# Kernel tuning notes

Hardware: AMD Instinct MI355X
Metric: run time of the kernel (lower is better)

The kernel has to match this reference:

```python
import jax, jax.numpy as jnp
import numpy as np

N = 30000        # nodes
E = 300000       # edges (before self-loops)
B = 300          # graphs
EMB = 64         # emb_dim (inner_dim overwritten to emb_dim in __init__)
HEADS = 4
OUT3 = 121       # hard-coded in conv3
H3 = 6           # heads of conv3
NCLS = 10
NVOC = 5000      # node token vocab for node_encoder
MAXD = 64        # max node depth for node_encoder


def _p(k, shape, scale=0.1):
    return scale * jax.random.normal(k, shape, dtype=jnp.float32)


def setup_inputs() -> dict:
    key = jax.random.key(0)
    ks = jax.random.split(key, 20)
    inp = {}
    inp["x"] = jax.random.randint(ks[0], (N, 1), 0, NVOC, dtype=jnp.int32)
    inp["node_depth"] = jax.random.randint(ks[1], (N, 1), 0, MAXD, dtype=jnp.int32)
    inp["edge_index"] = jax.random.randint(ks[2], (2, E), 0, N, dtype=jnp.int32)
    inp["batch"] = jnp.sort(jax.random.randint(ks[3], (N,), 0, B, dtype=jnp.int32))
    # node_encoder params (token emb + depth emb)
    inp["node_emb"] = _p(ks[4], (NVOC, EMB))
    inp["depth_emb"] = _p(ks[5], (MAXD, EMB))
    d1 = HEADS * EMB
    inp["w1"] = _p(ks[6], (EMB, d1))
    inp["as1"] = _p(ks[7], (HEADS, EMB))
    inp["ad1"] = _p(ks[8], (HEADS, EMB))
    inp["b1"] = jnp.zeros((d1,), jnp.float32)
    inp["w2"] = _p(ks[9], (d1, d1))
    inp["as2"] = _p(ks[10], (HEADS, EMB))
    inp["ad2"] = _p(ks[11], (HEADS, EMB))
    inp["b2"] = jnp.zeros((d1,), jnp.float32)
    d3 = H3 * OUT3
    inp["w3"] = _p(ks[12], (d1, d3))
    inp["as3"] = _p(ks[13], (H3, OUT3))
    inp["ad3"] = _p(ks[14], (H3, OUT3))
    inp["b3"] = jnp.zeros((d3,), jnp.float32)
    inp["wp"] = _p(ks[15], (OUT3, NCLS))
    inp["bp"] = jnp.zeros((NCLS,), jnp.float32)
    return inp


def gat_conv(x, W, a_src, a_dst, bias, src, dst, heads, out_dim):
    """PyG GATConv (concat=True, self-loops already in src/dst)."""
    n = x.shape[0]
    h = (x @ W).reshape(n, heads, out_dim)          # [N,H,D]
    es = (h * a_src).sum(-1)                        # [N,H] per-node src logits
    ed = (h * a_dst).sum(-1)                        # [N,H]
    e = jax.nn.leaky_relu(es[src] + ed[dst], 0.2)   # [E,H]
    # segment softmax over destination nodes (every node has a self-loop)
    m = jax.ops.segment_max(e, dst, num_segments=n)
    ex = jnp.exp(e - m[dst])
    s = jax.ops.segment_sum(ex, dst, num_segments=n)
    alpha = ex / (s[dst] + 1e-16)                   # [E,H]
    out = jax.ops.segment_sum(h[src] * alpha[:, :, None], dst, num_segments=n)
    return out.reshape(n, heads * out_dim) + bias


def reference(x, node_depth, edge_index, batch, node_emb, depth_emb,
              w1, as1, ad1, b1, w2, as2, ad2, b2, w3, as3, ad3, b3, wp, bp):
    n = x.shape[0]
    loops = jnp.arange(n, dtype=edge_index.dtype)
    src = jnp.concatenate([edge_index[0], loops])
    dst = jnp.concatenate([edge_index[1], loops])
    # node_encoder: token embedding + depth embedding
    h = node_emb[x[:, 0]] + depth_emb[node_depth.reshape(-1)]
    h = jax.nn.elu(gat_conv(h, w1, as1, ad1, b1, src, dst, HEADS, EMB))
    h = jax.nn.elu(gat_conv(h, w2, as2, ad2, b2, src, dst, HEADS, EMB))
    h = gat_conv(h, w3, as3, ad3, b3, src, dst, H3, OUT3)   # [N, 726]
    # global mean pool over graphs
    sums = jax.ops.segment_sum(h, batch, num_segments=B)
    cnt = jax.ops.segment_sum(jnp.ones((n,), h.dtype), batch, num_segments=B)
    g = sums / jnp.maximum(cnt, 1.0)[:, None]               # [B, 726]
    g = g.reshape(-1, H3, OUT3).mean(axis=1)                # [B, 121]
    return g @ wp + bp                                      # [B, NCLS]
```

## Files before the change

### kernel.cpp

```cpp
#include <hip/hip_runtime.h>
#include <hip/hip_bf16.h>
#include <math.h>

#define NN   30000
#define NE   300000
#define ETOT 330000
#define NB   300
#define EMB  64
#define D1   256
#define H1   4
#define H3   6
#define O3   121
#define D3   726
#define NQ   60
#define N3   72
#define NCLS 10
#define CAP  64
#define LDA  40

typedef __attribute__((ext_vector_type(8))) short short8;
typedef __attribute__((ext_vector_type(8))) unsigned short ushort8;
typedef __attribute__((ext_vector_type(4))) float floatx4;

static inline int ceil_div(int a, int b) { return (a + b - 1) / b; }

__device__ inline void split_bf16(float f, unsigned short& hi, unsigned short& lo) {
    __hip_bfloat16 h = __float2bfloat16(f);
    float fh = __bfloat162float(h);
    __hip_bfloat16 l = __float2bfloat16(f - fh);
    hi = __builtin_bit_cast(unsigned short, h);
    lo = __builtin_bit_cast(unsigned short, l);
}

__device__ inline float bf2f(unsigned short u) {
    return __builtin_bit_cast(float, (unsigned int)u << 16);
}

__device__ inline unsigned short f2bf(float f) {
    return __builtin_bit_cast(unsigned short, __float2bfloat16(f));
}

__device__ inline float lrelu(float v) { return v > 0.f ? v : 0.2f * v; }


__global__ void setup_kernel(const int* __restrict__ x, const int* __restrict__ dep,
                             const int* __restrict__ ei, const int* __restrict__ batch,
                             const float* __restrict__ nemb, const float* __restrict__ demb,
                             const float* __restrict__ w1, const float* __restrict__ w2,
                             const float* __restrict__ w3, const float* __restrict__ as3,
                             const float* __restrict__ ad3, const float* __restrict__ wp,
                             const float* __restrict__ b3,
                             unsigned short* __restrict__ H0hi, unsigned short* __restrict__ H0lo,
                             unsigned short* __restrict__ W1hi, unsigned short* __restrict__ W1lo,
                             unsigned short* __restrict__ W2b, unsigned short* __restrict__ W3b,
                             float* __restrict__ btv,
                             int* __restrict__ cnt, int* __restrict__ csr,
                             int* __restrict__ gs, int* __restrict__ ge) {
    int i = blockIdx.x * blockDim.x + threadIdx.x;
    if (i < NN * EMB) {
        int n = i >> 6, d = i & 63;
        float v = nemb[x[n] * EMB + d] + demb[dep[n] * EMB + d];
        split_bf16(v, H0hi[i], H0lo[i]);
    }
    if (i < ETOT) {
        int src, dst;
        if (i < NE) { src = ei[i]; dst = ei[NE + i]; }
        else        { src = i - NE; dst = src; }
        int slot = atomicAdd(&cnt[dst], 1);
        csr[dst * CAP + slot] = src;
    }
    if (i < NN) {
        int b = batch[i];
        if (i == 0 || batch[i - 1] != b) gs[b] = i;
        if (i == NN - 1 || batch[i + 1] != b) ge[b] = i + 1;
    }
    if (i < EMB * D1) {
        int k = i / D1, n = i % D1;
        unsigned short h, l;
        split_bf16(w1[i], h, l);
        W1hi[n * EMB + k] = h;
        W1lo[n * EMB + k] = l;
    }
    if (i < D1 * D1) {
        int k = i / D1, n = i % D1;
        W2b[n * D1 + k] = f2bf(w2[i]);
    }
    if (i < N3 * D1 * 8) {
        int oid = i >> 3, sub = i & 7;
        int n = oid / D1, k = oid % D1;
        const float* wrow = w3 + (size_t)k * D3;
        float acc = 0.f;
        if (n < NQ) {
            int h = n / NCLS, c = n % NCLS;
            const float* wr = wrow + h * O3;
            for (int j = sub; j < O3; j += 8) acc += wr[j] * wp[j * NCLS + c];
        } else if (n < NQ + H3) {
            int h = n - NQ;
            const float* wr = wrow + h * O3;
            for (int j = sub; j < O3; j += 8) acc += wr[j] * as3[h * O3 + j];
        } else {
            int h = n - NQ - H3;
            const float* wr = wrow + h * O3;
            for (int j = sub; j < O3; j += 8) acc += wr[j] * ad3[h * O3 + j];
        }
        acc += __shfl_xor(acc, 1);
        acc += __shfl_xor(acc, 2);
        acc += __shfl_xor(acc, 4);
        if (sub == 0) W3b[oid] = f2bf(acc);
    }
    if (i < NCLS * 8) {
        int c = i >> 3, sub = i & 7;
        float acc = 0.f;
        for (int k = sub; k < O3; k += 8) {
            float bs = 0.f;
            #pragma unroll
            for (int hh = 0; hh < H3; hh++) bs += b3[hh * O3 + k];
            acc += bs * wp[k * NCLS + c];
        }
        acc += __shfl_xor(acc, 1);
        acc += __shfl_xor(acc, 2);
        acc += __shfl_xor(acc, 4);
        if (sub == 0) btv[c] = acc;
    }
}


template <int MODE, bool SPLIT>
__global__ __launch_bounds__(256) void gemm_mfma_kernel(
    const unsigned short* __restrict__ Ahi, const unsigned short* __restrict__ Alo,
    const unsigned short* __restrict__ Bhi, const unsigned short* __restrict__ Blo,
    unsigned short* __restrict__ Cbf, unsigned short* __restrict__ Qb,
    float* __restrict__ es, float* __restrict__ ed,
    const float* __restrict__ as_, const float* __restrict__ ad_,
    int M, int K, int N) {
    __shared__ unsigned short sAh[128 * LDA], sBh[128 * LDA];
    __shared__ unsigned short sAl[SPLIT ? 128 * LDA : 1], sBl[SPLIT ? 128 * LDA : 1];
    int tid = threadIdx.x;
    int lane = tid & 63, wave = tid >> 6;
    int wr = (wave >> 1) * 64, wc = (wave & 1) * 64;
    int quad = lane >> 4, mr = lane & 15;
    int row0 = blockIdx.y * 128, col0 = blockIdx.x * 128;

    floatx4 zero = {0.f, 0.f, 0.f, 0.f};
    floatx4 acc[4][4];
    #pragma unroll
    for (int i = 0; i < 4; i++)
        #pragma unroll
        for (int j = 0; j < 4; j++) acc[i][j] = zero;

    for (int k0 = 0; k0 < K; k0 += 32) {
        #pragma unroll
        for (int ch = 0; ch < 2; ch++) {
            int linear = (ch * 256 + tid) * 8;
            int r = linear >> 5, c = linear & 31;
            uint4 vh, vl;
            int gr = row0 + r;
            if (gr < M) {
                vh = *(const uint4*)(Ahi + (size_t)gr * K + k0 + c);
                if (SPLIT) vl = *(const uint4*)(Alo + (size_t)gr * K + k0 + c);
            } else { vh = uint4{0, 0, 0, 0}; vl = uint4{0, 0, 0, 0}; }
            *(uint4*)&sAh[r * LDA + c] = vh;
            if (SPLIT) *(uint4*)&sAl[r * LDA + c] = vl;
            int gn = col0 + r;
            if (gn < N) {
                vh = *(const uint4*)(Bhi + (size_t)gn * K + k0 + c);
                if (SPLIT) vl = *(const uint4*)(Blo + (size_t)gn * K + k0 + c);
            } else { vh = uint4{0, 0, 0, 0}; vl = uint4{0, 0, 0, 0}; }
            *(uint4*)&sBh[r * LDA + c] = vh;
            if (SPLIT) *(uint4*)&sBl[r * LDA + c] = vl;
        }
        __syncthreads();

        short8 ah[4], al[4], bh[4], bl[4];
        #pragma unroll
        for (int i = 0; i < 4; i++) {
            int ar = wr + i * 16 + mr;
            ah[i] = *(const short8*)&sAh[ar * LDA + quad * 8];
            if (SPLIT) al[i] = *(const short8*)&sAl[ar * LDA + quad * 8];
            int br = wc + i * 16 + mr;
            bh[i] = *(const short8*)&sBh[br * LDA + quad * 8];
            if (SPLIT) bl[i] = *(const short8*)&sBl[br * LDA + quad * 8];
        }
        #pragma unroll
        for (int i = 0; i < 4; i++)
            #pragma unroll
            for (int j = 0; j < 4; j++) {
                acc[i][j] = __builtin_amdgcn_mfma_f32_16x16x32_bf16(ah[i], bh[j], acc[i][j], 0, 0, 0);
                if (SPLIT) {
                    acc[i][j] = __builtin_amdgcn_mfma_f32_16x16x32_bf16(ah[i], bl[j], acc[i][j], 0, 0, 0);
                    acc[i][j] = __builtin_amdgcn_mfma_f32_16x16x32_bf16(al[i], bh[j], acc[i][j], 0, 0, 0);
                }
            }
        __syncthreads();
    }

    #pragma unroll
    for (int i = 0; i < 4; i++) {
        #pragma unroll
        for (int j = 0; j < 4; j++) {
            int gc = col0 + wc + j * 16 + mr;
            if (gc >= N) continue;
            int gr0 = row0 + wr + i * 16 + quad * 4;
            #pragma unroll
            for (int r = 0; r < 4; r++) {
                int gr = gr0 + r;
                if (gr >= M) continue;
                float v = acc[i][j][r];
                if (MODE == 0) {
                    Cbf[(size_t)gr * D1 + gc] = f2bf(v);
                } else {
                    if (gc < NQ)            Qb[(size_t)gr * NQ + gc] = f2bf(v);
                    else if (gc < NQ + H3)  es[(size_t)gr * H3 + (gc - NQ)] = v;
                    else                    ed[(size_t)gr * H3 + (gc - NQ - H3)] = v;
                }
            }
        }
    }

    if (MODE == 0) {
        int hx = 2 * blockIdx.x + (wave & 1);
        float asr[4], adr[4];
        #pragma unroll
        for (int j = 0; j < 4; j++) {
            asr[j] = as_[hx * 64 + j * 16 + mr];
            adr[j] = ad_[hx * 64 + j * 16 + mr];
        }
        #pragma unroll
        for (int i = 0; i < 4; i++) {
            #pragma unroll
            for (int r = 0; r < 4; r++) {
                float ps = 0.f, pd = 0.f;
                #pragma unroll
                for (int j = 0; j < 4; j++) {
                    float v = acc[i][j][r];
                    ps += v * asr[j];
                    pd += v * adr[j];
                }
                #pragma unroll
                for (int m2 = 8; m2 >= 1; m2 >>= 1) {
                    ps += __shfl_xor(ps, m2);
                    pd += __shfl_xor(pd, m2);
                }
                int gr = row0 + wr + i * 16 + quad * 4 + r;
                if (mr == 0 && gr < M) {
                    es[gr * 4 + hx] = ps;
                    ed[gr * 4 + hx] = pd;
                }
            }
        }
    }
}


__global__ __launch_bounds__(256) void aggregate12_kernel(
    const unsigned short* __restrict__ P, const float* __restrict__ es,
    const float* __restrict__ ed, const int* __restrict__ cnt,
    const int* __restrict__ csr, const float* __restrict__ bias,
    unsigned short* __restrict__ outHi) {
    int wave = threadIdx.x >> 6, lane = threadIdx.x & 63;
    int wid = blockIdx.x * 4 + wave;
    int hi = lane >> 5;
    int fl = lane & 31;
    int hq = fl >> 3;
    int f0 = fl * 8;
    float bv[8];
    #pragma unroll
    for (int j = 0; j < 8; j++) bv[j] = bias[f0 + j];
    #pragma unroll 1
    for (int t = 0; t < 4; t++) {
        int dst = wid * 4 + t;
        int s0 = dst * CAP, s1 = s0 + cnt[dst];
        float edv = ed[dst * 4 + hq];
        float sum = 0.f;
        float acc[8];
        #pragma unroll
        for (int j = 0; j < 8; j++) acc[j] = 0.f;
        int s = s0;
        for (; s + 8 <= s1; s += 8) {
            int si[4]; float ev[4]; ushort8 pp[4];
            #pragma unroll
            for (int u = 0; u < 4; u++) si[u] = csr[s + 2 * u + hi];
            #pragma unroll
            for (int u = 0; u < 4; u++) {
                ev[u] = es[si[u] * 4 + hq] + edv;
                pp[u] = *(const ushort8*)(P + (size_t)si[u] * D1 + f0);
            }
            #pragma unroll
            for (int u = 0; u < 4; u++) {
                float e = __expf(lrelu(ev[u]));
                sum += e;
                #pragma unroll
                for (int j = 0; j < 8; j++) acc[j] += e * bf2f(pp[u][j]);
            }
        }
        for (; s + 4 <= s1; s += 4) {
            int si[2]; float ev[2]; ushort8 pp[2];
            #pragma unroll
            for (int u = 0; u < 2; u++) si[u] = csr[s + 2 * u + hi];
            #pragma unroll
            for (int u = 0; u < 2; u++) {
                ev[u] = es[si[u] * 4 + hq] + edv;
                pp[u] = *(const ushort8*)(P + (size_t)si[u] * D1 + f0);
            }
            #pragma unroll
            for (int u = 0; u < 2; u++) {
                float e = __expf(lrelu(ev[u]));
                sum += e;
                #pragma unroll
                for (int j = 0; j < 8; j++) acc[j] += e * bf2f(pp[u][j]);
            }
        }
        for (; s < s1; s += 2) {
            int idx = s + hi;
            bool v = idx < s1;
            int si = csr[v ? idx : s];
            float evv = es[si * 4 + hq] + edv;
            ushort8 p8 = *(const ushort8*)(P + (size_t)si * D1 + f0);
            float e = v ? __expf(lrelu(evv)) : 0.f;
            sum += e;
            #pragma unroll
            for (int j = 0; j < 8; j++) acc[j] += e * bf2f(p8[j]);
        }
        sum += __shfl_xor(sum, 32);
        #pragma unroll
        for (int j = 0; j < 8; j++) acc[j] += __shfl_xor(acc[j], 32);
        float inv = 1.f / sum;
        if (lane < 32) {
            ushort8 o8;
            #pragma unroll
            for (int j = 0; j < 8; j++) {
                float a = acc[j] * inv + bv[j];
                a = a > 0.f ? a : expm1f(a);
                o8[j] = f2bf(a);
            }
            *(ushort8*)(outHi + (size_t)dst * D1 + f0) = o8;
        }
    }
}


__global__ __launch_bounds__(256) void aggregate3q_kernel(
    const unsigned short* __restrict__ Qb, const float* __restrict__ es,
    const float* __restrict__ ed, const int* __restrict__ cnt,
    const int* __restrict__ csr, const int* __restrict__ batch,
    float* __restrict__ G,
    const int* __restrict__ gs, const int* __restrict__ ge,
    const float* __restrict__ btv, const float* __restrict__ bp,
    float* __restrict__ out, int* __restrict__ bar) {
    __shared__ int s_last;
    int wave = threadIdx.x >> 6, lane = threadIdx.x & 63;
    int wid = blockIdx.x * 4 + wave;
    bool act = lane < NQ;
    int h = act ? (lane / NCLS) : 0;
    int q = act ? lane : 0;
    #pragma unroll 1
    for (int t = 0; t < 4; t++) {
        int dst = wid * 4 + t;
        int b = batch[dst];
        int s0 = dst * CAP, s1 = s0 + cnt[dst];
        float edv = act ? ed[dst * H3 + h] : 0.f;
        float sum = 0.f, acc = 0.f;
        int s = s0;
        for (; s + 8 <= s1; s += 8) {
            int si[8];
            #pragma unroll
            for (int u = 0; u < 8; u++) si[u] = csr[s + u];
            float vv[8], qq[8];
            #pragma unroll
            for (int u = 0; u < 8; u++) {
                vv[u] = es[si[u] * H3 + h] + edv;
                qq[u] = bf2f(Qb[(size_t)si[u] * NQ + q]);
            }
            #pragma unroll
            for (int u = 0; u < 8; u++) {
                float e = __expf(lrelu(vv[u]));
                sum += e;
                acc += e * qq[u];
            }
        }
        for (; s + 2 <= s1; s += 2) {
            int sa = csr[s], sb = csr[s + 1];
            float va = es[sa * H3 + h] + edv;
            float vb = es[sb * H3 + h] + edv;
            float qa = bf2f(Qb[(size_t)sa * NQ + q]);
            float qb = bf2f(Qb[(size_t)sb * NQ + q]);
            float ea = __expf(lrelu(va));
            float eb = __expf(lrelu(vb));
            sum += ea + eb;
            acc += ea * qa + eb * qb;
        }
        for (; s < s1; s++) {
            int sa = csr[s];
            float va = es[sa * H3 + h] + edv;
            float qa = bf2f(Qb[(size_t)sa * NQ + q]);
            float ea = __expf(lrelu(va));
            sum += ea;
            acc += ea * qa;
        }
        acc *= 1.f / sum;
        float av = act ? acc : 0.f;
        float tot = av;
        #pragma unroll
        for (int h2 = 1; h2 < H3; h2++) tot += __shfl(av, lane + h2 * NCLS);
        if (lane < NCLS) atomicAdd(&G[b * NCLS + lane], tot);
    }

    asm volatile("s_waitcnt vmcnt(0)" ::: "memory");
    __syncthreads();
    if (threadIdx.x == 0) {
        int old = atomicAdd(bar, 1);
        int last = (old == (int)gridDim.x - 1) ? 1 : 0;
        if (last) __threadfence();
        s_last = last;
    }
    __syncthreads();
    if (s_last) {
        for (int i = threadIdx.x; i < NB * NCLS; i += blockDim.x) {
            int b = i / NCLS, c = i % NCLS;
            int cntn = ge[b] - gs[b];
            float o = bp[c];
            if (cntn > 0)
                o += G[i] / (6.f * (float)cntn) + btv[c] * (1.f / 6.f);
            out[i] = o;
        }
    }
}


extern "C" void kernel_launch(void* const* d_in, const int* in_sizes, int n_in,
                              void* d_out, int out_size, void* d_ws, size_t ws_size,
                              hipStream_t stream) {
    const int* x     = (const int*)d_in[0];
    const int* dep   = (const int*)d_in[1];
    const int* ei    = (const int*)d_in[2];
    const int* batch = (const int*)d_in[3];
    const float* nemb = (const float*)d_in[4];
    const float* demb = (const float*)d_in[5];
    const float* w1  = (const float*)d_in[6];
    const float* as1 = (const float*)d_in[7];
    const float* ad1 = (const float*)d_in[8];
    const float* b1  = (const float*)d_in[9];
    const float* w2  = (const float*)d_in[10];
    const float* as2 = (const float*)d_in[11];
    const float* ad2 = (const float*)d_in[12];
    const float* b2  = (const float*)d_in[13];
    const float* w3  = (const float*)d_in[14];
    const float* as3 = (const float*)d_in[15];
    const float* ad3 = (const float*)d_in[16];
    const float* b3  = (const float*)d_in[17];
    const float* wp  = (const float*)d_in[18];
    const float* bp  = (const float*)d_in[19];
    float* out = (float*)d_out;

    char* ws = (char*)d_ws;
    size_t off = 0;
    auto alloc = [&](size_t bytes) -> void* {
        void* p = ws + off;
        off += (bytes + 255) & ~(size_t)255;
        return p;
    };
    unsigned short* Hb   = (unsigned short*)alloc((size_t)NN * D1 * 2);
    unsigned short* H0lo = (unsigned short*)alloc((size_t)NN * EMB * 2);
    unsigned short* W1hi = (unsigned short*)alloc((size_t)D1 * EMB * 2);
    unsigned short* W1lo = (unsigned short*)alloc((size_t)D1 * EMB * 2);
    unsigned short* W2b  = (unsigned short*)alloc((size_t)D1 * D1 * 2);
    unsigned short* W3b  = (unsigned short*)alloc((size_t)N3 * D1 * 2);
    unsigned short* Pb   = (unsigned short*)alloc((size_t)NN * D1 * 2);
    unsigned short* Qb   = (unsigned short*)alloc(((size_t)NN * NQ + 64) * 2);
    float* es   = (float*)alloc((size_t)NN * 6 * 4);
    float* ed   = (float*)alloc((size_t)NN * 6 * 4);
    int* csr    = (int*)alloc((size_t)NN * CAP * 4);
    float* btv  = (float*)alloc((size_t)NCLS * 4);
    char* zstart = ws + off;
    float* G    = (float*)alloc((size_t)NB * NCLS * 4);
    int* gs     = (int*)alloc((size_t)NB * 4);
    int* ge     = (int*)alloc((size_t)NB * 4);
    int* cnt    = (int*)alloc((size_t)NN * 4);
    int* bar    = (int*)alloc((size_t)64 * 4);
    size_t zbytes = (size_t)((ws + off) - zstart);

    hipMemsetAsync(zstart, 0, zbytes, stream);

    setup_kernel<<<ceil_div(NN * EMB, 256), 256, 0, stream>>>(
        x, dep, ei, batch, nemb, demb, w1, w2, w3, as3, ad3, wp, b3,
        Hb, H0lo, W1hi, W1lo, W2b, W3b, btv, cnt, csr, gs, ge);

    gemm_mfma_kernel<0, true><<<dim3(2, ceil_div(NN, 128)), 256, 0, stream>>>(
        Hb, H0lo, W1hi, W1lo, Pb, nullptr, es, ed, as1, ad1, NN, EMB, D1);
    aggregate12_kernel<<<NN / 16, 256, 0, stream>>>(Pb, es, ed, cnt, csr, b1, Hb);

    gemm_mfma_kernel<0, false><<<dim3(2, ceil_div(NN, 128)), 256, 0, stream>>>(
        Hb, nullptr, W2b, nullptr, Pb, nullptr, es, ed, as2, ad2, NN, D1, D1);
    aggregate12_kernel<<<NN / 16, 256, 0, stream>>>(Pb, es, ed, cnt, csr, b2, Hb);

    gemm_mfma_kernel<1, false><<<dim3(1, ceil_div(NN, 128)), 256, 0, stream>>>(
        Hb, nullptr, W3b, nullptr, nullptr, Qb, es, ed, nullptr, nullptr, NN, D1, N3);

    aggregate3q_kernel<<<NN / 16, 256, 0, stream>>>(
        Qb, es, ed, cnt, csr, batch, G, gs, ge, btv, bp, out, bar);
}
```

Measured before the change: 278.1 us.

## Prefetch next node's CSR indices into lanes and shuffle-broadcast neighbor ids

In both aggregation kernels, each lane now loads one neighbor index of the destination node's CSR row into a register, and per-edge source ids are obtained by lane shuffles instead of repeated global loads. The degree, ed value and index row for the next destination node are prefetched during the current one, so that latency overlaps with the gather work. The three unrolled remainder loops are replaced by one masked loop of 8 edges, which removes tail code but spends loads and exps on masked lanes for the last partial block.

```diff
diff --git a/kernel.cpp b/kernel.cpp
--- a/kernel.cpp
+++ b/kernel.cpp
@@ -266,60 +266,49 @@
     float bv[8];
     #pragma unroll
     for (int j = 0; j < 8; j++) bv[j] = bias[f0 + j];
+
+    int dstN = wid * 4;
+    int degN = cnt[dstN];
+    float edvN = ed[dstN * 4 + hq];
+    int sivN = csr[dstN * CAP + (fl < degN ? fl : degN - 1)];
+
     #pragma unroll 1
     for (int t = 0; t < 4; t++) {
-        int dst = wid * 4 + t;
-        int s0 = dst * CAP, s1 = s0 + cnt[dst];
-        float edv = ed[dst * 4 + hq];
+        int dst = dstN;
+        int deg = degN;
+        float edv = edvN;
+        int siv = sivN;
+        if (t < 3) {
+            dstN = dst + 1;
+            degN = cnt[dstN];
+            edvN = ed[dstN * 4 + hq];
+            sivN = csr[dstN * CAP + (fl < degN ? fl : degN - 1)];
+        }
         float sum = 0.f;
         float acc[8];
         #pragma unroll
         for (int j = 0; j < 8; j++) acc[j] = 0.f;
-        int s = s0;
-        for (; s + 8 <= s1; s += 8) {
-            int si[4]; float ev[4]; ushort8 pp[4];
-            #pragma unroll
-            for (int u = 0; u < 4; u++) si[u] = csr[s + 2 * u + hi];
+        #pragma unroll 1
+        for (int sb = 0; sb < deg; sb += 8) {
+            float ev[4]; ushort8 pp[4]; bool vm[4];
             #pragma unroll
             for (int u = 0; u < 4; u++) {
-                ev[u] = es[si[u] * 4 + hq] + edv;
-                pp[u] = *(const ushort8*)(P + (size_t)si[u] * D1 + f0);
+                int e = sb + 2 * u + hi;
+                bool v = e < deg;
+                vm[u] = v;
+                int si;
+                if (e < 32) si = __shfl(siv, v ? e : 0);
+                else        si = csr[dst * CAP + (v ? e : 0)];
+                ev[u] = es[si * 4 + hq] + edv;
+                pp[u] = *(const ushort8*)(P + (size_t)si * D1 + f0);
             }
             #pragma unroll
             for (int u = 0; u < 4; u++) {
-                float e = __expf(lrelu(ev[u]));
+                float e = vm[u] ? __expf(lrelu(ev[u])) : 0.f;
                 sum += e;
                 #pragma unroll
                 for (int j = 0; j < 8; j++) acc[j] += e * bf2f(pp[u][j]);
             }
-        }
-        for (; s + 4 <= s1; s += 4) {
-            int si[2]; float ev[2]; ushort8 pp[2];
-            #pragma unroll
-            for (int u = 0; u < 2; u++) si[u] = csr[s + 2 * u + hi];
-            #pragma unroll
-            for (int u = 0; u < 2; u++) {
-                ev[u] = es[si[u] * 4 + hq] + edv;
-                pp[u] = *(const ushort8*)(P + (size_t)si[u] * D1 + f0);
-            }
-            #pragma unroll
-            for (int u = 0; u < 2; u++) {
-                float e = __expf(lrelu(ev[u]));
-                sum += e;
-                #pragma unroll
-                for (int j = 0; j < 8; j++) acc[j] += e * bf2f(pp[u][j]);
-            }
-        }
-        for (; s < s1; s += 2) {
-            int idx = s + hi;
-            bool v = idx < s1;
-            int si = csr[v ? idx : s];
-            float evv = es[si * 4 + hq] + edv;
-            ushort8 p8 = *(const ushort8*)(P + (size_t)si * D1 + f0);
-            float e = v ? __expf(lrelu(evv)) : 0.f;
-            sum += e;
-            #pragma unroll
-            for (int j = 0; j < 8; j++) acc[j] += e * bf2f(p8[j]);
         }
         sum += __shfl_xor(sum, 32);
         #pragma unroll
@@ -353,49 +342,47 @@
     bool act = lane < NQ;
     int h = act ? (lane / NCLS) : 0;
     int q = act ? lane : 0;
+    int el = lane & 31;
+
+    int dstN = wid * 4;
+    int degN = cnt[dstN];
+    float edvN = act ? ed[dstN * H3 + h] : 0.f;
+    int sivN = csr[dstN * CAP + (el < degN ? el : degN - 1)];
+
     #pragma unroll 1
     for (int t = 0; t < 4; t++) {
-        int dst = wid * 4 + t;
+        int dst = dstN;
+        int deg = degN;
+        float edv = edvN;
+        int siv = sivN;
+        if (t < 3) {
+            dstN = dst + 1;
+            degN = cnt[dstN];
+            edvN = act ? ed[dstN * H3 + h] : 0.f;
+            sivN = csr[dstN * CAP + (el < degN ? el : degN - 1)];
+        }
         int b = batch[dst];
-        int s0 = dst * CAP, s1 = s0 + cnt[dst];
-        float edv = act ? ed[dst * H3 + h] : 0.f;
         float sum = 0.f, acc = 0.f;
-        int s = s0;
-        for (; s + 8 <= s1; s += 8) {
-            int si[8];
-            #pragma unroll
-            for (int u = 0; u < 8; u++) si[u] = csr[s + u];
-            float vv[8], qq[8];
+        #pragma unroll 1
+        for (int sb = 0; sb < deg; sb += 8) {
+            float vv[8], qq[8]; bool vm[8];
             #pragma unroll
             for (int u = 0; u < 8; u++) {
-                vv[u] = es[si[u] * H3 + h] + edv;
-                qq[u] = bf2f(Qb[(size_t)si[u] * NQ + q]);
+                int e = sb + u;
+                bool v = e < deg;
+                vm[u] = v;
+                int si;
+                if (e < 32) si = __shfl(siv, v ? e : 0);
+                else        si = csr[dst * CAP + (v ? e : 0)];
+                vv[u] = es[si * H3 + h] + edv;
+                qq[u] = bf2f(Qb[(size_t)si * NQ + q]);
             }
             #pragma unroll
             for (int u = 0; u < 8; u++) {
-                float e = __expf(lrelu(vv[u]));
+                float e = vm[u] ? __expf(lrelu(vv[u])) : 0.f;
                 sum += e;
                 acc += e * qq[u];
             }
-        }
-        for (; s + 2 <= s1; s += 2) {
-            int sa = csr[s], sb = csr[s + 1];
-            float va = es[sa * H3 + h] + edv;
-            float vb = es[sb * H3 + h] + edv;
-            float qa = bf2f(Qb[(size_t)sa * NQ + q]);
-            float qb = bf2f(Qb[(size_t)sb * NQ + q]);
-            float ea = __expf(lrelu(va));
-            float eb = __expf(lrelu(vb));
-            sum += ea + eb;
-            acc += ea * qa + eb * qb;
-        }
-        for (; s < s1; s++) {
-            int sa = csr[s];
-            float va = es[sa * H3 + h] + edv;
-            float qa = bf2f(Qb[(size_t)sa * NQ + q]);
-            float ea = __expf(lrelu(va));
-            sum += ea;
-            acc += ea * qa;
         }
         acc *= 1.f / sum;
         float av = act ? acc : 0.f;
```

After: 302.5 us. 8.8% more time.
